# Kernel optimization log

Measured on AMD Instinct MI355X. Metric: run time of the kernel, lower is better.

The kernel has to match this reference:

```python
import jax, jax.numpy as jnp
import numpy as np

B, TQ, TK, DK, DV = 64, 1024, 1024, 64, 64


def setup_inputs() -> dict:
    key = jax.random.key(0)
    kq, kk, kv, km = jax.random.split(key, 4)
    q = jax.random.normal(kq, (B, TQ, DK), dtype=jnp.float32)
    k = jax.random.normal(kk, (B, TK, DK), dtype=jnp.float32)
    v = jax.random.normal(kv, (B, TK, DV), dtype=jnp.float32)
    mask = jax.random.randint(km, (B, TQ, TK), 0, 2).astype(jnp.int32)
    return {"q": q, "k": k, "v": v, "mask": mask}


def reference(q, k, v, mask):
    # attn = q @ k^T / sqrt(d_k)   -> [B, TQ, TK]
    temper = jnp.sqrt(jnp.asarray(q.shape[-1], dtype=jnp.float32))
    attn = jnp.einsum('bqd,bkd->bqk', q, k) / temper
    # mask-add: -1e9 where mask == 0
    mmask = -1e9 * (1.0 - mask.astype(jnp.float32))
    attn = attn + mmask
    attn = jax.nn.softmax(attn, axis=-1)
    # dropout rate is 0.0 -> identity
    out = jnp.einsum('bqk,bkd->bqd', attn, v)
    return (out, attn)
```

## Files before the change

kernel.cpp:

```cpp
#include <hip/hip_runtime.h>
#include <hip/hip_bf16.h>


#define B_   64
#define TQ_  1024
#define TK_  1024
#define DD   64

typedef short short8 __attribute__((ext_vector_type(8)));
typedef float f32x4 __attribute__((ext_vector_type(4)));

#define PLW    68
#define PL_U32 (16 * PLW)

#define QB_OFF  (0u)
#define KB_OFF  (8u << 20)
#define VT_OFF  (16u << 20)
#define MB_OFF  (24u << 20)
#define WS_NEED (32u << 20)

__device__ __forceinline__ unsigned cvt2(float a, float b) {
    __hip_bfloat162 h = __float22bfloat162_rn(make_float2(a, b));
    unsigned u; __builtin_memcpy(&u, &h, 4); return u;
}
__device__ __forceinline__ short cvt1(float a) {
    __hip_bfloat16 h = __float2bfloat16(a);
    short s; __builtin_memcpy(&s, &h, 2); return s;
}

union Frag { short8 s; unsigned u[4]; };

__global__ __launch_bounds__(256) void prep_kernel(
    const float* __restrict__ qg, const float* __restrict__ kg,
    const float* __restrict__ vg, const int* __restrict__ maskg,
    unsigned char* __restrict__ ws)
{
    const int t = threadIdx.x;
    const int gid = blockIdx.x;
    if (gid < 1024) {
        __shared__ short tl[64][72];
        const int b  = gid >> 4;
        const int k0 = (gid & 15) * 64;
        const float* vb = vg + (size_t)b * TK_ * DD;
        short* ob = (short*)(ws + VT_OFF) + (size_t)b * DD * TK_;
        #pragma unroll
        for (int i = 0; i < 4; ++i) {
            const int row = i * 16 + (t >> 4);
            const int d   = (t & 15) * 4;
            const float4 x = *(const float4*)(vb + (size_t)(k0 + row) * DD + d);
            tl[d + 0][row] = cvt1(x.x); tl[d + 1][row] = cvt1(x.y);
            tl[d + 2][row] = cvt1(x.z); tl[d + 3][row] = cvt1(x.w);
        }
        __syncthreads();
        #pragma unroll
        for (int p = 0; p < 2; ++p) {
            const int d = p * 32 + (t >> 3);
            const uint4 val = *(const uint4*)&tl[d][(t & 7) * 8];
            *(uint4*)(ob + (size_t)d * TK_ + k0 + (t & 7) * 8) = val;
        }
    } else if (gid < 1024 + 8192) {
        const int widx = (gid - 1024) * 256 + t;
        const int4* mp = (const int4*)(maskg + (size_t)widx * 32);
        unsigned bits = 0;
        #pragma unroll
        for (int i = 0; i < 8; ++i) {
            const int4 x = mp[i];
            bits |= (unsigned)(x.x & 1) << (4 * i)
                 |  (unsigned)(x.y & 1) << (4 * i + 1)
                 |  (unsigned)(x.z & 1) << (4 * i + 2)
                 |  (unsigned)(x.w & 1) << (4 * i + 3);
        }
        ((unsigned*)(ws + MB_OFF))[widx] = bits;
    } else if (gid < 1024 + 8192 + 2048) {
        const int i8 = (gid - 1024 - 8192) * 256 + t;
        const float* p = qg + (size_t)i8 * 8;
        const float4 x = *(const float4*)p, y = *(const float4*)(p + 4);
        uint4 o;
        o.x = cvt2(0.125f * x.x, 0.125f * x.y); o.y = cvt2(0.125f * x.z, 0.125f * x.w);
        o.z = cvt2(0.125f * y.x, 0.125f * y.y); o.w = cvt2(0.125f * y.z, 0.125f * y.w);
        ((uint4*)(ws + QB_OFF))[i8] = o;
    } else {
        const int i8 = (gid - 1024 - 8192 - 2048) * 256 + t;
        const float* p = kg + (size_t)i8 * 8;
        const float4 x = *(const float4*)p, y = *(const float4*)(p + 4);
        uint4 o;
        o.x = cvt2(x.x, x.y); o.y = cvt2(x.z, x.w);
        o.z = cvt2(y.x, y.y); o.w = cvt2(y.z, y.w);
        ((uint4*)(ws + KB_OFF))[i8] = o;
    }
}

__global__ __launch_bounds__(256, 4) void attn_bf16_kernel(
    const unsigned char* __restrict__ ws,
    float* __restrict__ outg, float* __restrict__ attng)
{
    __shared__ __align__(16) unsigned lds[4 * PL_U32];
    __shared__ float red[128];

    const int t    = threadIdx.x;
    const int wave = t >> 6, lane = t & 63;
    const int quad = lane >> 4, n16 = lane & 15;
    const int b    = blockIdx.y;
    const int q0   = blockIdx.x * 16;
    const int kbase = wave * 256;

    const short*    Qb = (const short*)(ws + QB_OFF);
    const short*    Kb = (const short*)(ws + KB_OFF);
    const short*    Vt = (const short*)(ws + VT_OFF);
    const unsigned* Mb = (const unsigned*)(ws + MB_OFF);

    unsigned* pl = lds + wave * PL_U32;

    const unsigned* mrow = Mb + ((size_t)(b * TQ_ + q0 + n16)) * 32 + wave * 8;
    const uint4 mw0 = *(const uint4*)(mrow);
    const uint4 mw1 = *(const uint4*)(mrow + 4);

    const short* qp = Qb + ((size_t)(b * TQ_ + q0 + n16)) * DD + quad * 8;
    Frag qf0, qf1;
    qf0.s = *(const short8*)(qp);
    qf1.s = *(const short8*)(qp + 32);

    const short* vrow = Vt + (size_t)b * DD * TK_ + (size_t)n16 * TK_ + kbase + quad * 8;
    Frag vf[4];
    #pragma unroll
    for (int dg = 0; dg < 4; ++dg)
        vf[dg].s = *(const short8*)(vrow + (size_t)(dg * 16) * TK_);

    const short* kbp = Kb + (size_t)(b * TK_ + kbase) * DD;
    Frag kf[16][2];
    #pragma unroll
    for (int kt = 0; kt < 16; ++kt) {
        const short* kp = kbp + (size_t)(kt * 16 + n16) * DD + quad * 8;
        kf[kt][0].s = *(const short8*)(kp);
        kf[kt][1].s = *(const short8*)(kp + 32);
    }

    float s_reg[64];
    const unsigned mwa[8] = {mw0.x, mw0.y, mw0.z, mw0.w, mw1.x, mw1.y, mw1.z, mw1.w};
    #pragma unroll
    for (int kt = 0; kt < 16; ++kt) {
        f32x4 acc = {0.f, 0.f, 0.f, 0.f};
        acc = __builtin_amdgcn_mfma_f32_16x16x32_bf16(kf[kt][0].s, qf0.s, acc, 0, 0, 0);
        acc = __builtin_amdgcn_mfma_f32_16x16x32_bf16(kf[kt][1].s, qf1.s, acc, 0, 0, 0);
        const unsigned m4 = (mwa[kt >> 1] >> (((kt & 1) << 4) | (quad << 2))) & 15u;
        s_reg[kt * 4 + 0] = acc[0] + ((m4 & 1u) ? 0.f : -1e9f);
        s_reg[kt * 4 + 1] = acc[1] + ((m4 & 2u) ? 0.f : -1e9f);
        s_reg[kt * 4 + 2] = acc[2] + ((m4 & 4u) ? 0.f : -1e9f);
        s_reg[kt * 4 + 3] = acc[3] + ((m4 & 8u) ? 0.f : -1e9f);
    }

    float m8[8];
    #pragma unroll
    for (int j = 0; j < 8; ++j) m8[j] = s_reg[j];
    #pragma unroll
    for (int i = 8; i < 64; i += 8)
        #pragma unroll
        for (int j = 0; j < 8; ++j) m8[j] = fmaxf(m8[j], s_reg[i + j]);
    float m = fmaxf(fmaxf(fmaxf(m8[0], m8[1]), fmaxf(m8[2], m8[3])),
                    fmaxf(fmaxf(m8[4], m8[5]), fmaxf(m8[6], m8[7])));
    m = fmaxf(m, __shfl_xor(m, 16));
    m = fmaxf(m, __shfl_xor(m, 32));
    if (lane < 16) red[wave * 16 + n16] = m;
    __syncthreads();
    const float gm = fmaxf(fmaxf(red[n16], red[16 + n16]),
                           fmaxf(red[32 + n16], red[48 + n16]));
    float l0 = 0.f, l1 = 0.f, l2 = 0.f, l3 = 0.f;
    #pragma unroll
    for (int i = 0; i < 16; ++i) {
        const float p0 = __expf(s_reg[4*i+0] - gm);
        const float p1 = __expf(s_reg[4*i+1] - gm);
        const float p2 = __expf(s_reg[4*i+2] - gm);
        const float p3 = __expf(s_reg[4*i+3] - gm);
        s_reg[4*i+0] = p0; s_reg[4*i+1] = p1;
        s_reg[4*i+2] = p2; s_reg[4*i+3] = p3;
        l0 += p0; l1 += p1; l2 += p2; l3 += p3;
    }
    float lsum = (l0 + l1) + (l2 + l3);
    lsum += __shfl_xor(lsum, 16);
    lsum += __shfl_xor(lsum, 32);
    if (lane < 16) red[64 + wave * 16 + n16] = lsum;
    __syncthreads();
    const float inv = 1.f / (red[64 + n16] + red[80 + n16] +
                             red[96 + n16] + red[112 + n16]);
    #pragma unroll
    for (int i = 0; i < 64; ++i) s_reg[i] *= inv;

    float* ab = attng + ((size_t)(b * TQ_ + q0 + n16)) * TK_ + kbase + quad * 4;
    #pragma unroll
    for (int kt = 0; kt < 16; ++kt)
        *(float4*)(ab + kt * 16) = make_float4(s_reg[kt*4+0], s_reg[kt*4+1],
                                               s_reg[kt*4+2], s_reg[kt*4+3]);
    #pragma unroll
    for (int kt = 0; kt < 8; ++kt) {
        uint2 u;
        u.x = cvt2(s_reg[kt*4+0], s_reg[kt*4+1]);
        u.y = cvt2(s_reg[kt*4+2], s_reg[kt*4+3]);
        *(uint2*)&pl[n16 * PLW + kt * 8 + quad * 2] = u;
    }

    f32x4 oacc[4];
    #pragma unroll
    for (int dg = 0; dg < 4; ++dg) oacc[dg] = (f32x4){0.f, 0.f, 0.f, 0.f};

    #pragma unroll
    for (int c = 0; c < 4; ++c) {
        Frag cur[4];
        #pragma unroll
        for (int dg = 0; dg < 4; ++dg) cur[dg] = vf[dg];
        #pragma unroll
        for (int dg = 0; dg < 4; ++dg)
            vf[dg].s = *(const short8*)(vrow + (size_t)(dg * 16) * TK_ + (c + 1) * 32);
        Frag pf;
        pf.s = *(const short8*)&pl[n16 * PLW + c * 16 + quad * 4];
        #pragma unroll
        for (int dg = 0; dg < 4; ++dg)
            oacc[dg] = __builtin_amdgcn_mfma_f32_16x16x32_bf16(cur[dg].s, pf.s, oacc[dg], 0, 0, 0);
    }

    #pragma unroll
    for (int kt = 8; kt < 16; ++kt) {
        uint2 u;
        u.x = cvt2(s_reg[kt*4+0], s_reg[kt*4+1]);
        u.y = cvt2(s_reg[kt*4+2], s_reg[kt*4+3]);
        *(uint2*)&pl[n16 * PLW + (kt - 8) * 8 + quad * 2] = u;
    }

    #pragma unroll
    for (int c = 0; c < 4; ++c) {
        Frag cur[4];
        #pragma unroll
        for (int dg = 0; dg < 4; ++dg) cur[dg] = vf[dg];
        if (c < 3) {
            #pragma unroll
            for (int dg = 0; dg < 4; ++dg)
                vf[dg].s = *(const short8*)(vrow + (size_t)(dg * 16) * TK_ + (c + 5) * 32);
        }
        Frag pf;
        pf.s = *(const short8*)&pl[n16 * PLW + c * 16 + quad * 4];
        #pragma unroll
        for (int dg = 0; dg < 4; ++dg)
            oacc[dg] = __builtin_amdgcn_mfma_f32_16x16x32_bf16(cur[dg].s, pf.s, oacc[dg], 0, 0, 0);
    }

    float* ow = (float*)pl;
    #pragma unroll
    for (int dg = 0; dg < 4; ++dg)
        *(f32x4*)&ow[n16 * PLW + dg * 16 + quad * 4] = oacc[dg];
    __syncthreads();
    {
        const int row = t >> 4, col = (t & 15) * 4;
        const float* base = (const float*)lds;
        float4 o = make_float4(0.f, 0.f, 0.f, 0.f);
        #pragma unroll
        for (int w = 0; w < 4; ++w) {
            const float4 x = *(const float4*)(base + w * PL_U32 + row * PLW + col);
            o.x += x.x; o.y += x.y; o.z += x.z; o.w += x.w;
        }
        *(float4*)(outg + ((size_t)(b * TQ_ + q0 + row)) * DD + col) = o;
    }
}

#define PSTR 264
#define FWVS (16 * PSTR)

__global__ __launch_bounds__(256, 3) void attn_fallback_kernel(
    const float* __restrict__ qg, const float* __restrict__ kg,
    const float* __restrict__ vg, const int* __restrict__ maskg,
    float* __restrict__ outg, float* __restrict__ attng)
{
    __shared__ __align__(16) short lds[4 * FWVS];
    __shared__ float red[128];

    const int t    = threadIdx.x;
    const int wave = t >> 6, lane = t & 63;
    const int quad = lane >> 4, n16 = lane & 15;
    const int b    = blockIdx.y;
    const int q0   = blockIdx.x * 16;
    const int kbase = wave * 256;

    short* pw = lds + wave * FWVS;

    Frag aq[2];
    {
        const float* qp = qg + ((size_t)(b * TQ_ + q0 + n16)) * DD + quad * 8;
        #pragma unroll
        for (int f = 0; f < 2; ++f) {
            float4 x = *(const float4*)(qp + f * 32);
            float4 y = *(const float4*)(qp + f * 32 + 4);
            aq[f].u[0] = cvt2(0.125f * x.x, 0.125f * x.y);
            aq[f].u[1] = cvt2(0.125f * x.z, 0.125f * x.w);
            aq[f].u[2] = cvt2(0.125f * y.x, 0.125f * y.y);
            aq[f].u[3] = cvt2(0.125f * y.z, 0.125f * y.w);
        }
    }

    float s_reg[64];
    const float* kbp  = kg + (size_t)b * TK_ * DD;
    const int*   mrow = maskg + ((size_t)(b * TQ_ + q0 + n16)) * TK_ + kbase + quad * 4;
    #pragma unroll
    for (int h = 0; h < 2; ++h) {
        int4 mk[8];
        #pragma unroll
        for (int i = 0; i < 8; ++i)
            mk[i] = *(const int4*)(mrow + (h * 8 + i) * 16);
        #pragma unroll
        for (int i = 0; i < 8; ++i) {
            const int kt = h * 8 + i;
            const float* kp = kbp + (size_t)(kbase + kt * 16 + n16) * DD + quad * 8;
            Frag bk[2];
            #pragma unroll
            for (int f = 0; f < 2; ++f) {
                float4 x = *(const float4*)(kp + f * 32);
                float4 y = *(const float4*)(kp + f * 32 + 4);
                bk[f].u[0] = cvt2(x.x, x.y); bk[f].u[1] = cvt2(x.z, x.w);
                bk[f].u[2] = cvt2(y.x, y.y); bk[f].u[3] = cvt2(y.z, y.w);
            }
            f32x4 acc = {0.f, 0.f, 0.f, 0.f};
            acc = __builtin_amdgcn_mfma_f32_16x16x32_bf16(bk[0].s, aq[0].s, acc, 0, 0, 0);
            acc = __builtin_amdgcn_mfma_f32_16x16x32_bf16(bk[1].s, aq[1].s, acc, 0, 0, 0);
            s_reg[kt * 4 + 0] = acc[0] + (mk[i].x ? 0.f : -1e9f);
            s_reg[kt * 4 + 1] = acc[1] + (mk[i].y ? 0.f : -1e9f);
            s_reg[kt * 4 + 2] = acc[2] + (mk[i].z ? 0.f : -1e9f);
            s_reg[kt * 4 + 3] = acc[3] + (mk[i].w ? 0.f : -1e9f);
        }
    }

    const float* vb0 = vg + (size_t)b * TK_ * DD + (size_t)(kbase + quad * 8) * DD + n16;
    float vraw[32];
    #pragma unroll
    for (int u = 0; u < 32; ++u)
        vraw[u] = vb0[(size_t)(u & 7) * DD + (u >> 3) * 16];

    float m8[8];
    #pragma unroll
    for (int j = 0; j < 8; ++j) m8[j] = s_reg[j];
    #pragma unroll
    for (int i = 8; i < 64; i += 8)
        #pragma unroll
        for (int j = 0; j < 8; ++j) m8[j] = fmaxf(m8[j], s_reg[i + j]);
    float m = fmaxf(fmaxf(fmaxf(m8[0], m8[1]), fmaxf(m8[2], m8[3])),
                    fmaxf(fmaxf(m8[4], m8[5]), fmaxf(m8[6], m8[7])));
    m = fmaxf(m, __shfl_xor(m, 16));
    m = fmaxf(m, __shfl_xor(m, 32));
    if (lane < 16) red[wave * 16 + n16] = m;
    __syncthreads();
    const float gm = fmaxf(fmaxf(red[n16], red[16 + n16]),
                           fmaxf(red[32 + n16], red[48 + n16]));
    float l0 = 0.f, l1 = 0.f, l2 = 0.f, l3 = 0.f;
    #pragma unroll
    for (int i = 0; i < 16; ++i) {
        const float p0 = __expf(s_reg[4*i+0] - gm);
        const float p1 = __expf(s_reg[4*i+1] - gm);
        const float p2 = __expf(s_reg[4*i+2] - gm);
        const float p3 = __expf(s_reg[4*i+3] - gm);
        s_reg[4*i+0] = p0; s_reg[4*i+1] = p1;
        s_reg[4*i+2] = p2; s_reg[4*i+3] = p3;
        l0 += p0; l1 += p1; l2 += p2; l3 += p3;
    }
    float lsum = (l0 + l1) + (l2 + l3);
    lsum += __shfl_xor(lsum, 16);
    lsum += __shfl_xor(lsum, 32);
    if (lane < 16) red[64 + wave * 16 + n16] = lsum;
    __syncthreads();
    const float inv = 1.f / (red[64 + n16] + red[80 + n16] +
                             red[96 + n16] + red[112 + n16]);
    #pragma unroll
    for (int i = 0; i < 64; ++i) s_reg[i] *= inv;

    float* ab = attng + ((size_t)(b * TQ_ + q0 + n16)) * TK_ + kbase + quad * 4;
    #pragma unroll
    for (int kt = 0; kt < 16; ++kt)
        *(float4*)(ab + kt * 16) = make_float4(s_reg[kt*4+0], s_reg[kt*4+1],
                                               s_reg[kt*4+2], s_reg[kt*4+3]);
    #pragma unroll
    for (int kt = 0; kt < 16; ++kt) {
        uint2 u;
        u.x = cvt2(s_reg[kt*4+0], s_reg[kt*4+1]);
        u.y = cvt2(s_reg[kt*4+2], s_reg[kt*4+3]);
        *(uint2*)(pw + n16 * PSTR + kt * 16 + quad * 4) = u;
    }

    f32x4 oacc[4];
    #pragma unroll
    for (int dg = 0; dg < 4; ++dg) oacc[dg] = (f32x4){0.f, 0.f, 0.f, 0.f};

    #pragma unroll
    for (int c = 0; c < 8; ++c) {
        unsigned va16[16];
        #pragma unroll
        for (int dg = 0; dg < 4; ++dg)
            #pragma unroll
            for (int w = 0; w < 4; ++w)
                va16[dg * 4 + w] = cvt2(vraw[dg * 8 + 2 * w], vraw[dg * 8 + 2 * w + 1]);
        if (c < 7) {
            #pragma unroll
            for (int u = 0; u < 32; ++u)
                vraw[u] = vb0[(size_t)((c + 1) * 32 + (u & 7)) * DD + (u >> 3) * 16];
        }
        Frag pf;
        pf.s = *(const short8*)(pw + n16 * PSTR + c * 32 + quad * 8);
        #pragma unroll
        for (int dg = 0; dg < 4; ++dg) {
            Frag af;
            af.u[0] = va16[dg*4+0]; af.u[1] = va16[dg*4+1];
            af.u[2] = va16[dg*4+2]; af.u[3] = va16[dg*4+3];
            oacc[dg] = __builtin_amdgcn_mfma_f32_16x16x32_bf16(af.s, pf.s, oacc[dg], 0, 0, 0);
        }
    }

    float* ow = (float*)pw;
    #pragma unroll
    for (int dg = 0; dg < 4; ++dg)
        *(f32x4*)&ow[n16 * 68 + dg * 16 + quad * 4] = oacc[dg];
    __syncthreads();
    {
        const int row = t >> 4, col = (t & 15) * 4;
        const float* base = (const float*)lds;
        float4 o = make_float4(0.f, 0.f, 0.f, 0.f);
        #pragma unroll
        for (int w = 0; w < 4; ++w) {
            const float4 x = *(const float4*)(base + w * (FWVS / 2) + row * 68 + col);
            o.x += x.x; o.y += x.y; o.z += x.z; o.w += x.w;
        }
        *(float4*)(outg + ((size_t)(b * TQ_ + q0 + row)) * DD + col) = o;
    }
}

extern "C" void kernel_launch(void* const* d_in, const int* in_sizes, int n_in,
                              void* d_out, int out_size, void* d_ws, size_t ws_size,
                              hipStream_t stream) {
    const float* q    = (const float*)d_in[0];
    const float* k    = (const float*)d_in[1];
    const float* v    = (const float*)d_in[2];
    const int*   mask = (const int*)d_in[3];

    float* out  = (float*)d_out;
    float* attn = out + (size_t)B_ * TQ_ * DD;

    if (ws_size >= (size_t)WS_NEED && d_ws != nullptr) {
        unsigned char* ws = (unsigned char*)d_ws;
        prep_kernel<<<dim3(13312), 256, 0, stream>>>(q, k, v, mask, ws);
        attn_bf16_kernel<<<dim3(TQ_ / 16, B_), 256, 0, stream>>>(ws, out, attn);
    } else {
        attn_fallback_kernel<<<dim3(TQ_ / 16, B_), 256, 0, stream>>>(q, k, v, mask, out, attn);
    }
}
```

Before: 615.7 us.

## Pack mask bits with wave ballots and halve K-fragment register footprint

The mask packing now uses wave-wide ballots, so each lane reads one coalesced int4 and lane 0 writes 32 bytes, replacing the per-thread strided 128-byte reads. The packed bit layout changes to match, so the attention kernel indexes mask bits differently. K fragments are loaded in two halves of 8 tiles, with the second half loaded inside the first MFMA loop. V fragment loads move after the softmax. Together these are meant to cut register pressure and improve occupancy, at the risk of exposing load latency.

Measured after the change: 630.5 us. +2.4%, slower.

```diff
diff --git a/kernel.cpp b/kernel.cpp
--- a/kernel.cpp
+++ b/kernel.cpp
@@ -59,18 +59,27 @@
             *(uint4*)(ob + (size_t)d * TK_ + k0 + (t & 7) * 8) = val;
         }
     } else if (gid < 1024 + 8192) {
-        const int widx = (gid - 1024) * 256 + t;
-        const int4* mp = (const int4*)(maskg + (size_t)widx * 32);
-        unsigned bits = 0;
+        const int blk = gid - 1024;
+        const int w = t >> 6, l = t & 63;
+        unsigned* mb = (unsigned*)(ws + MB_OFF);
         #pragma unroll
         for (int i = 0; i < 8; ++i) {
-            const int4 x = mp[i];
-            bits |= (unsigned)(x.x & 1) << (4 * i)
-                 |  (unsigned)(x.y & 1) << (4 * i + 1)
-                 |  (unsigned)(x.z & 1) << (4 * i + 2)
-                 |  (unsigned)(x.w & 1) << (4 * i + 3);
-        }
-        ((unsigned*)(ws + MB_OFF))[widx] = bits;
+            const int g = blk * 32 + w * 8 + i;
+            const int4 x = *(const int4*)(maskg + (size_t)g * 256 + 4 * l);
+            const unsigned long long b0 = __ballot(x.x & 1);
+            const unsigned long long b1 = __ballot(x.y & 1);
+            const unsigned long long b2 = __ballot(x.z & 1);
+            const unsigned long long b3 = __ballot(x.w & 1);
+            if (l == 0) {
+                uint4 o0, o1;
+                o0.x = (unsigned)b0; o0.y = (unsigned)(b0 >> 32);
+                o0.z = (unsigned)b1; o0.w = (unsigned)(b1 >> 32);
+                o1.x = (unsigned)b2; o1.y = (unsigned)(b2 >> 32);
+                o1.z = (unsigned)b3; o1.w = (unsigned)(b3 >> 32);
+                *(uint4*)(mb + (size_t)g * 8)     = o0;
+                *(uint4*)(mb + (size_t)g * 8 + 4) = o1;
+            }
+        }
     } else if (gid < 1024 + 8192 + 2048) {
         const int i8 = (gid - 1024 - 8192) * 256 + t;
         const float* p = qg + (size_t)i8 * 8;
@@ -111,42 +120,52 @@
 
     unsigned* pl = lds + wave * PL_U32;
 
-    const unsigned* mrow = Mb + ((size_t)(b * TQ_ + q0 + n16)) * 32 + wave * 8;
-    const uint4 mw0 = *(const uint4*)(mrow);
-    const uint4 mw1 = *(const uint4*)(mrow + 4);
+    const unsigned* mg = Mb + ((size_t)(b * TQ_ + q0 + n16) * 4 + wave) * 8;
+    const uint4 M0 = *(const uint4*)(mg);
+    const uint4 M1 = *(const uint4*)(mg + 4);
 
     const short* qp = Qb + ((size_t)(b * TQ_ + q0 + n16)) * DD + quad * 8;
     Frag qf0, qf1;
     qf0.s = *(const short8*)(qp);
     qf1.s = *(const short8*)(qp + 32);
 
-    const short* vrow = Vt + (size_t)b * DD * TK_ + (size_t)n16 * TK_ + kbase + quad * 8;
-    Frag vf[4];
-    #pragma unroll
-    for (int dg = 0; dg < 4; ++dg)
-        vf[dg].s = *(const short8*)(vrow + (size_t)(dg * 16) * TK_);
-
     const short* kbp = Kb + (size_t)(b * TK_ + kbase) * DD;
-    Frag kf[16][2];
-    #pragma unroll
-    for (int kt = 0; kt < 16; ++kt) {
+    Frag kf[8][2];
+    #pragma unroll
+    for (int kt = 0; kt < 8; ++kt) {
         const short* kp = kbp + (size_t)(kt * 16 + n16) * DD + quad * 8;
         kf[kt][0].s = *(const short8*)(kp);
         kf[kt][1].s = *(const short8*)(kp + 32);
     }
+    __builtin_amdgcn_sched_barrier(0);
 
     float s_reg[64];
-    const unsigned mwa[8] = {mw0.x, mw0.y, mw0.z, mw0.w, mw1.x, mw1.y, mw1.z, mw1.w};
-    #pragma unroll
-    for (int kt = 0; kt < 16; ++kt) {
+    #pragma unroll
+    for (int kt = 0; kt < 8; ++kt) {
         f32x4 acc = {0.f, 0.f, 0.f, 0.f};
         acc = __builtin_amdgcn_mfma_f32_16x16x32_bf16(kf[kt][0].s, qf0.s, acc, 0, 0, 0);
         acc = __builtin_amdgcn_mfma_f32_16x16x32_bf16(kf[kt][1].s, qf1.s, acc, 0, 0, 0);
-        const unsigned m4 = (mwa[kt >> 1] >> (((kt & 1) << 4) | (quad << 2))) & 15u;
-        s_reg[kt * 4 + 0] = acc[0] + ((m4 & 1u) ? 0.f : -1e9f);
-        s_reg[kt * 4 + 1] = acc[1] + ((m4 & 2u) ? 0.f : -1e9f);
-        s_reg[kt * 4 + 2] = acc[2] + ((m4 & 4u) ? 0.f : -1e9f);
-        s_reg[kt * 4 + 3] = acc[3] + ((m4 & 8u) ? 0.f : -1e9f);
+        {
+            const short* kp = kbp + (size_t)((kt + 8) * 16 + n16) * DD + quad * 8;
+            kf[kt][0].s = *(const short8*)(kp);
+            kf[kt][1].s = *(const short8*)(kp + 32);
+        }
+        const unsigned sh = (unsigned)(kt * 4) + (unsigned)quad;
+        s_reg[kt * 4 + 0] = acc[0] + (((M0.x >> sh) & 1u) ? 0.f : -1e9f);
+        s_reg[kt * 4 + 1] = acc[1] + (((M0.z >> sh) & 1u) ? 0.f : -1e9f);
+        s_reg[kt * 4 + 2] = acc[2] + (((M1.x >> sh) & 1u) ? 0.f : -1e9f);
+        s_reg[kt * 4 + 3] = acc[3] + (((M1.z >> sh) & 1u) ? 0.f : -1e9f);
+    }
+    #pragma unroll
+    for (int kt = 8; kt < 16; ++kt) {
+        f32x4 acc = {0.f, 0.f, 0.f, 0.f};
+        acc = __builtin_amdgcn_mfma_f32_16x16x32_bf16(kf[kt - 8][0].s, qf0.s, acc, 0, 0, 0);
+        acc = __builtin_amdgcn_mfma_f32_16x16x32_bf16(kf[kt - 8][1].s, qf1.s, acc, 0, 0, 0);
+        const unsigned sh = (unsigned)((kt - 8) * 4) + (unsigned)quad;
+        s_reg[kt * 4 + 0] = acc[0] + (((M0.y >> sh) & 1u) ? 0.f : -1e9f);
+        s_reg[kt * 4 + 1] = acc[1] + (((M0.w >> sh) & 1u) ? 0.f : -1e9f);
+        s_reg[kt * 4 + 2] = acc[2] + (((M1.y >> sh) & 1u) ? 0.f : -1e9f);
+        s_reg[kt * 4 + 3] = acc[3] + (((M1.w >> sh) & 1u) ? 0.f : -1e9f);
     }
 
     float m8[8];
@@ -184,6 +203,12 @@
                              red[96 + n16] + red[112 + n16]);
     #pragma unroll
     for (int i = 0; i < 64; ++i) s_reg[i] *= inv;
+
+    const short* vrow = Vt + (size_t)b * DD * TK_ + (size_t)n16 * TK_ + kbase + quad * 8;
+    Frag vf[4];
+    #pragma unroll
+    for (int dg = 0; dg < 4; ++dg)
+        vf[dg].s = *(const short8*)(vrow + (size_t)(dg * 16) * TK_);
 
     float* ab = attng + ((size_t)(b * TQ_ + q0 + n16)) * TK_ + kbase + quad * 4;
     #pragma unroll
```
